# Optimization experiments

Measured on AMD Instinct MI355X. Metric: run time of the kernel, lower is better.

Reference implementation:

```python
import jax, jax.numpy as jnp
import numpy as np

B, T, N = 16, 1024, 512

def setup_inputs() -> dict:
    key = jax.random.key(0)
    ks = jax.random.split(key, 6)
    scale = 1.0 / np.sqrt(N)
    x = jax.random.normal(ks[0], (B, T, N), dtype=jnp.float32)
    Wq = jax.random.normal(ks[1], (N, N), dtype=jnp.float32) * scale
    Wk = jax.random.normal(ks[2], (N, N), dtype=jnp.float32) * scale
    Wv = jax.random.normal(ks[3], (N, N), dtype=jnp.float32) * scale
    Wp = jax.random.normal(ks[4], (N, N), dtype=jnp.float32) * scale
    bp = jnp.zeros((N,), dtype=jnp.float32)
    return {"x": x, "Wq": Wq, "Wk": Wk, "Wv": Wv, "Wp": Wp, "bp": bp}

def reference(x, Wq, Wk, Wv, Wp, bp):
    # x: [B, T, N]; conv1d(k=1) over node channels == 'oi,bit->bot' on x^T [B,N,T]
    xt = jnp.swapaxes(x, -1, -2)                     # [B, N, T]
    q = jnp.einsum('oi,bit->bot', Wq, xt)            # [B, N, T]
    k = jnp.einsum('oi,bit->bot', Wk, xt)
    v = jnp.einsum('oi,bit->bot', Wv, xt)
    n = x.shape[-1]
    attn = jnp.einsum('bnt,bmt->bnm', q, k) * (n ** -0.5)  # [B, N, N]
    attn = jax.nn.softmax(attn, axis=-1)
    px = jnp.einsum('bnm,bmt->bnt', attn, v)         # [B, N, T]
    px = jnp.swapaxes(px, -1, -2)                    # [B, T, N]
    out = jnp.einsum('btn,on->bto', px, Wp) + bp     # Linear(N,N)
    return out
```

## Files before the change

kernel.cpp:

```cpp
#include <hip/hip_runtime.h>
#include <stdint.h>

#define BB 16
#define TT 1024
#define NN 512

typedef unsigned short u16;
typedef __bf16 bf16_t;
typedef bf16_t bf16x8 __attribute__((ext_vector_type(8)));
typedef float f32x4 __attribute__((ext_vector_type(4)));

struct alignas(8) U16x4 { u16 x, y, z, w; };
struct alignas(16) F32x4 { float x, y, z, w; };

__device__ __forceinline__ u16 f2bf(float f) {
    union { float f; uint32_t u; } v; v.f = f;
    uint32_t r = v.u + 0x7fffu + ((v.u >> 16) & 1u);
    return (u16)(r >> 16);
}

__device__ __forceinline__ void gload_lds16(const void* g, void* l) {
    __builtin_amdgcn_global_load_lds(
        (const __attribute__((address_space(1))) void*)g,
        (__attribute__((address_space(3))) void*)l, 16, 0, 0);
}

__device__ __forceinline__ void xcd_swizzle(int gx, int gy, int& bx, int& by) {
    const int nwg  = gx * gy;
    const int orig = by * gx + bx;
    const int q = nwg >> 3, r = nwg & 7;
    const int xcd = orig & 7, loc = orig >> 3;
    const int swz = (xcd < r ? xcd * (q + 1) : r * (q + 1) + (xcd - r) * q) + loc;
    bx = swz % gx;
    by = swz / gx;
}

__global__ __launch_bounds__(256)
void cvt_x(const float* __restrict__ x, u16* __restrict__ xb, u16* __restrict__ xT)
{
    __shared__ u16 tile[64][70];
    const int b  = blockIdx.z;
    const int t0 = blockIdx.x * 64;
    const int n0 = blockIdx.y * 64;
    const int i  = threadIdx.x;
#pragma unroll
    for (int rep = 0; rep < 4; rep++) {
        const int lin = rep * 256 + i;
        const int r = lin >> 4, c4 = (lin & 15) * 4;
        const long src = ((long)(b * TT + t0 + r)) * NN + n0 + c4;
        F32x4 f = *(const F32x4*)&x[src];
        U16x4 u;
        u.x = f2bf(f.x); u.y = f2bf(f.y); u.z = f2bf(f.z); u.w = f2bf(f.w);
        *(U16x4*)&xb[src] = u;
        tile[r][c4] = u.x; tile[r][c4 + 1] = u.y; tile[r][c4 + 2] = u.z; tile[r][c4 + 3] = u.w;
    }
    __syncthreads();
#pragma unroll
    for (int rep = 0; rep < 4; rep++) {
        const int lin = rep * 256 + i;
        const int n = lin >> 4, t4 = (lin & 15) * 4;
        U16x4 u;
        u.x = tile[t4][n]; u.y = tile[t4 + 1][n]; u.z = tile[t4 + 2][n]; u.w = tile[t4 + 3][n];
        *(U16x4*)&xT[((long)(b * NN + n0 + n)) * TT + t0 + t4] = u;
    }
}

__global__ __launch_bounds__(256)
void cvt_w(const float* __restrict__ Wq, const float* __restrict__ Wk,
           const float* __restrict__ Wv, const float* __restrict__ Wp,
           u16* __restrict__ wb)
{
    __shared__ u16 tile[64][70];
    const int z  = blockIdx.z;
    const int r0 = blockIdx.x * 64;
    const int c0 = blockIdx.y * 64;
    const int i  = threadIdx.x;
    const float* src = (z == 0) ? Wq : (z == 1) ? Wk : (z == 2) ? Wv : Wp;
    u16* dst = wb + z * 262144;
    if (z != 2) {
#pragma unroll
        for (int rep = 0; rep < 4; rep++) {
            const int lin = rep * 256 + i;
            const int r = lin >> 4, c4 = (lin & 15) * 4;
            F32x4 f = *(const F32x4*)&src[(r0 + r) * 512 + c0 + c4];
            U16x4 u;
            u.x = f2bf(f.x); u.y = f2bf(f.y); u.z = f2bf(f.z); u.w = f2bf(f.w);
            *(U16x4*)&dst[(r0 + r) * 512 + c0 + c4] = u;
        }
    } else {
#pragma unroll
        for (int rep = 0; rep < 4; rep++) {
            const int lin = rep * 256 + i;
            const int r = lin >> 4, c4 = (lin & 15) * 4;
            F32x4 f = *(const F32x4*)&src[(r0 + r) * 512 + c0 + c4];
            tile[r][c4]     = f2bf(f.x); tile[r][c4 + 1] = f2bf(f.y);
            tile[r][c4 + 2] = f2bf(f.z); tile[r][c4 + 3] = f2bf(f.w);
        }
        __syncthreads();
#pragma unroll
        for (int rep = 0; rep < 4; rep++) {
            const int lin = rep * 256 + i;
            const int n = lin >> 4, t4 = (lin & 15) * 4;
            U16x4 u;
            u.x = tile[t4][n]; u.y = tile[t4 + 1][n]; u.z = tile[t4 + 2][n]; u.w = tile[t4 + 3][n];
            *(U16x4*)&dst[(c0 + n) * 512 + r0 + t4] = u;
        }
    }
}

template<int MODE>
__global__ __launch_bounds__(256)
void gemm_nt(const u16* __restrict__ Ag, const u16* __restrict__ Bg,
             void* __restrict__ Cg, const float* __restrict__ bias,
             int Nc, int K, int lda, int ldb,
             long sA, long sB, long sC)
{
    const u16* A  = Ag + (long)blockIdx.z * sA;
    const u16* Bt = Bg + (long)blockIdx.z * sB;

    __shared__ u16 As[2][4096];
    __shared__ u16 Bs[2][4096];

    int bx = blockIdx.x, by = blockIdx.y;
    xcd_swizzle(gridDim.x, gridDim.y, bx, by);

    const int tid  = threadIdx.x;
    const int wave = tid >> 6;
    const int lane = tid & 63;
    const int arow0 = by * 128;
    const int brow0 = bx * 128;
    const int wr = (wave >> 1) * 64;
    const int wc = (wave & 1) * 64;

    const int srow = tid >> 2;
    const int sf   = ((srow >> 1) & 3) << 4;
    const int gcol = ((tid & 3) << 4) ^ sf;
    const char* Asrc = (const char*)A  + (long)(arow0 + srow) * lda * 2 + gcol;
    const char* Bsrc = (const char*)Bt + (long)(brow0 + srow) * ldb * 2 + gcol;
    const long rstepA = (long)64 * lda * 2;
    const long rstepB = (long)64 * ldb * 2;

    f32x4 zero = {0.f, 0.f, 0.f, 0.f};
    f32x4 acc[4][4];
#pragma unroll
    for (int i = 0; i < 4; i++)
#pragma unroll
        for (int j = 0; j < 4; j++) acc[i][j] = zero;

    const int kTiles = K >> 5;

    auto stage = [&](int buf, int kt) {
        const long kb = (long)kt * 64;
        char* ad = (char*)As + buf * 8192 + tid * 16;
        char* bd = (char*)Bs + buf * 8192 + tid * 16;
        gload_lds16(Asrc + kb,          ad);
        gload_lds16(Bsrc + kb,          bd);
        gload_lds16(Asrc + rstepA + kb, ad + 4096);
        gload_lds16(Bsrc + rstepB + kb, bd + 4096);
    };

    stage(0, 0);
    int cur = 0;
    const int kbyte = (lane >> 4) << 4;
    const int rA = lane & 15;

    for (int kt = 0; kt < kTiles; ++kt) {
        if (kt + 1 < kTiles) {
            stage(cur ^ 1, kt + 1);
            asm volatile("s_waitcnt vmcnt(4)" ::: "memory");
        } else {
            asm volatile("s_waitcnt vmcnt(0)" ::: "memory");
        }
        __builtin_amdgcn_s_barrier();
        asm volatile("" ::: "memory");

        bf16x8 av[4], bv[4];
        const char* as = (const char*)As + cur * 8192;
        const char* bs = (const char*)Bs + cur * 8192;
#pragma unroll
        for (int m = 0; m < 4; m++) {
            const int row = wr + m * 16 + rA;
            av[m] = *(const bf16x8*)(as + row * 64 + (kbyte ^ (((row >> 1) & 3) << 4)));
        }
#pragma unroll
        for (int n = 0; n < 4; n++) {
            const int row = wc + n * 16 + rA;
            bv[n] = *(const bf16x8*)(bs + row * 64 + (kbyte ^ (((row >> 1) & 3) << 4)));
        }
#pragma unroll
        for (int m = 0; m < 4; m++)
#pragma unroll
            for (int n = 0; n < 4; n++)
                acc[m][n] = __builtin_amdgcn_mfma_f32_16x16x32_bf16(av[m], bv[n], acc[m][n], 0, 0, 0);

        asm volatile("" ::: "memory");
        __builtin_amdgcn_s_barrier();
        cur ^= 1;
    }

    const int r0 = (lane >> 4) << 2;
    const int cl = lane & 15;
#pragma unroll
    for (int m = 0; m < 4; m++) {
        const long gm = (long)arow0 + wr + m * 16 + r0;
#pragma unroll
        for (int n = 0; n < 4; n++) {
            const long gn = (long)brow0 + wc + n * 16 + cl;
            if (MODE == 0) {
                u16* O = (u16*)Cg + blockIdx.z * sC;
#pragma unroll
                for (int r = 0; r < 4; r++)
                    O[(gm + r) * Nc + gn] = f2bf(acc[m][n][r]);
            } else {
                float* O = (float*)Cg + blockIdx.z * sC;
                const float bb = (MODE == 3) ? bias[gn] : 0.f;
#pragma unroll
                for (int r = 0; r < 4; r++)
                    O[(gm + r) * Nc + gn] = acc[m][n][r] + bb;
            }
        }
    }
}

__global__ __launch_bounds__(256)
void softmax_rows(float* __restrict__ S)
{
    const long r = blockIdx.x;
    float* row = S + r * 512;
    const int t = threadIdx.x;
    const int lane = t & 63, wave = t >> 6;
    const float scale = 0.04419417382415922f;

    float a = row[t] * scale;
    float b = row[t + 256] * scale;

    float m = fmaxf(a, b);
#pragma unroll
    for (int o = 32; o; o >>= 1) m = fmaxf(m, __shfl_xor(m, o, 64));

    __shared__ float red[8];
    if (lane == 0) red[wave] = m;
    __syncthreads();
    m = fmaxf(fmaxf(red[0], red[1]), fmaxf(red[2], red[3]));

    float e0 = __expf(a - m), e1 = __expf(b - m);
    float s = e0 + e1;
#pragma unroll
    for (int o = 32; o; o >>= 1) s += __shfl_xor(s, o, 64);
    if (lane == 0) red[wave + 4] = s;
    __syncthreads();
    s = red[4] + red[5] + red[6] + red[7];
    const float inv = 1.f / s;

    u16* P = (u16*)row;
    P[t]       = f2bf(e0 * inv);
    P[t + 256] = f2bf(e1 * inv);
}

extern "C" void kernel_launch(void* const* d_in, const int* in_sizes, int n_in,
                              void* d_out, int out_size, void* d_ws, size_t ws_size,
                              hipStream_t stream)
{
    (void)in_sizes; (void)n_in; (void)out_size; (void)ws_size;
    const float* x  = (const float*)d_in[0];
    const float* Wq = (const float*)d_in[1];
    const float* Wk = (const float*)d_in[2];
    const float* Wv = (const float*)d_in[3];
    const float* Wp = (const float*)d_in[4];
    const float* bp = (const float*)d_in[5];
    float* out = (float*)d_out;

    char* ws = (char*)d_ws;
    size_t o = 0;
    auto alloc = [&](size_t bytes) {
        char* p = ws + o;
        o = (o + bytes + 255) & ~(size_t)255;
        return p;
    };
    u16* xb = (u16*)alloc((size_t)BB * TT * NN * 2);
    u16* xT = (u16*)alloc((size_t)BB * NN * TT * 2);
    u16* wb = (u16*)alloc((size_t)4 * NN * NN * 2);
    u16* G  = (u16*)alloc((size_t)BB * NN * NN * 2);
    u16* H  = (u16*)alloc((size_t)BB * NN * NN * 2);
    float* S = (float*)alloc((size_t)BB * NN * NN * 4);
    u16* R  = (u16*)alloc((size_t)BB * NN * NN * 2);
    u16* px = (u16*)alloc((size_t)BB * TT * NN * 2);

    const u16* wqb  = wb;
    const u16* wkb  = wb + 1 * 262144;
    const u16* wvtb = wb + 2 * 262144;
    const u16* wpb  = wb + 3 * 262144;
    const long NSQ = (long)NN * NN;

    cvt_x<<<dim3(16, 8, 16), dim3(256), 0, stream>>>(x, xb, xT);
    cvt_w<<<dim3(8, 8, 4),  dim3(256), 0, stream>>>(Wq, Wk, Wv, Wp, wb);

    const dim3 blk(256);

    gemm_nt<0><<<dim3(4, 4, 16), blk, 0, stream>>>(xT, xT, G, nullptr,
        NN, TT, TT, TT, (long)NN * TT, (long)NN * TT, NSQ);

    gemm_nt<0><<<dim3(4, 4, 16), blk, 0, stream>>>(wqb, G, H, nullptr,
        NN, NN, NN, NN, 0, NSQ, NSQ);

    gemm_nt<2><<<dim3(4, 4, 16), blk, 0, stream>>>(H, wkb, S, nullptr,
        NN, NN, NN, NN, NSQ, 0, NSQ);

    softmax_rows<<<dim3(BB * NN), blk, 0, stream>>>(S);

    gemm_nt<0><<<dim3(4, 4, 16), blk, 0, stream>>>((const u16*)S, wvtb, R, nullptr,
        NN, NN, 1024, NN, (long)NN * 1024, 0, NSQ);

    gemm_nt<0><<<dim3(4, 8, 16), blk, 0, stream>>>(xb, R, px, nullptr,
        NN, NN, NN, NN, (long)TT * NN, NSQ, (long)TT * NN);

    gemm_nt<3><<<dim3(4, 128, 1), blk, 0, stream>>>(px, wpb, out, bp,
        NN, NN, NN, NN, 0, 0, 0);
}
```

Measured before the change: 199.4 us.

## Fold output projection into per-batch weight chain, triple-buffer GEMM, fuse conversions

Result: faster. 195.3 us (-2.0%).

```diff
diff --git a/kernel.cpp b/kernel.cpp
--- a/kernel.cpp
+++ b/kernel.cpp
@@ -36,65 +36,27 @@
 }
 
 __global__ __launch_bounds__(256)
-void cvt_x(const float* __restrict__ x, u16* __restrict__ xb, u16* __restrict__ xT)
+void cvt_fused(const float* __restrict__ x,
+               const float* __restrict__ Wq, const float* __restrict__ Wk,
+               const float* __restrict__ Wv, const float* __restrict__ Wp,
+               u16* __restrict__ xb, u16* __restrict__ xT, u16* __restrict__ wb)
 {
     __shared__ u16 tile[64][70];
-    const int b  = blockIdx.z;
-    const int t0 = blockIdx.x * 64;
-    const int n0 = blockIdx.y * 64;
-    const int i  = threadIdx.x;
-#pragma unroll
-    for (int rep = 0; rep < 4; rep++) {
-        const int lin = rep * 256 + i;
-        const int r = lin >> 4, c4 = (lin & 15) * 4;
-        const long src = ((long)(b * TT + t0 + r)) * NN + n0 + c4;
-        F32x4 f = *(const F32x4*)&x[src];
-        U16x4 u;
-        u.x = f2bf(f.x); u.y = f2bf(f.y); u.z = f2bf(f.z); u.w = f2bf(f.w);
-        *(U16x4*)&xb[src] = u;
-        tile[r][c4] = u.x; tile[r][c4 + 1] = u.y; tile[r][c4 + 2] = u.z; tile[r][c4 + 3] = u.w;
-    }
-    __syncthreads();
-#pragma unroll
-    for (int rep = 0; rep < 4; rep++) {
-        const int lin = rep * 256 + i;
-        const int n = lin >> 4, t4 = (lin & 15) * 4;
-        U16x4 u;
-        u.x = tile[t4][n]; u.y = tile[t4 + 1][n]; u.z = tile[t4 + 2][n]; u.w = tile[t4 + 3][n];
-        *(U16x4*)&xT[((long)(b * NN + n0 + n)) * TT + t0 + t4] = u;
-    }
-}
-
-__global__ __launch_bounds__(256)
-void cvt_w(const float* __restrict__ Wq, const float* __restrict__ Wk,
-           const float* __restrict__ Wv, const float* __restrict__ Wp,
-           u16* __restrict__ wb)
-{
-    __shared__ u16 tile[64][70];
-    const int z  = blockIdx.z;
-    const int r0 = blockIdx.x * 64;
-    const int c0 = blockIdx.y * 64;
-    const int i  = threadIdx.x;
-    const float* src = (z == 0) ? Wq : (z == 1) ? Wk : (z == 2) ? Wv : Wp;
-    u16* dst = wb + z * 262144;
-    if (z != 2) {
+    const int i = threadIdx.x;
+    if (blockIdx.z < 16) {
+        const int b  = blockIdx.z;
+        const int t0 = blockIdx.x * 64;
+        const int n0 = blockIdx.y * 64;
 #pragma unroll
         for (int rep = 0; rep < 4; rep++) {
             const int lin = rep * 256 + i;
             const int r = lin >> 4, c4 = (lin & 15) * 4;
-            F32x4 f = *(const F32x4*)&src[(r0 + r) * 512 + c0 + c4];
+            const long src = ((long)(b * TT + t0 + r)) * NN + n0 + c4;
+            F32x4 f = *(const F32x4*)&x[src];
             U16x4 u;
             u.x = f2bf(f.x); u.y = f2bf(f.y); u.z = f2bf(f.z); u.w = f2bf(f.w);
-            *(U16x4*)&dst[(r0 + r) * 512 + c0 + c4] = u;
-        }
-    } else {
-#pragma unroll
-        for (int rep = 0; rep < 4; rep++) {
-            const int lin = rep * 256 + i;
-            const int r = lin >> 4, c4 = (lin & 15) * 4;
-            F32x4 f = *(const F32x4*)&src[(r0 + r) * 512 + c0 + c4];
-            tile[r][c4]     = f2bf(f.x); tile[r][c4 + 1] = f2bf(f.y);
-            tile[r][c4 + 2] = f2bf(f.z); tile[r][c4 + 3] = f2bf(f.w);
+            *(U16x4*)&xb[src] = u;
+            tile[r][c4] = u.x; tile[r][c4 + 1] = u.y; tile[r][c4 + 2] = u.z; tile[r][c4 + 3] = u.w;
         }
         __syncthreads();
 #pragma unroll
@@ -103,7 +65,42 @@
             const int n = lin >> 4, t4 = (lin & 15) * 4;
             U16x4 u;
             u.x = tile[t4][n]; u.y = tile[t4 + 1][n]; u.z = tile[t4 + 2][n]; u.w = tile[t4 + 3][n];
-            *(U16x4*)&dst[(c0 + n) * 512 + r0 + t4] = u;
+            *(U16x4*)&xT[((long)(b * NN + n0 + n)) * TT + t0 + t4] = u;
+        }
+    } else {
+        const int idx = (blockIdx.z - 16) * 128 + blockIdx.y * 16 + blockIdx.x;
+        const int w = idx >> 6, wt = idx & 63;
+        const int r0 = (wt >> 3) * 64, c0 = (wt & 7) * 64;
+        const float* src = (w == 0) ? Wq : (w == 1) ? Wk : (w == 2) ? Wv : Wp;
+        u16* dst = wb + w * 262144;
+        if (w != 2) {
+#pragma unroll
+            for (int rep = 0; rep < 4; rep++) {
+                const int lin = rep * 256 + i;
+                const int r = lin >> 4, c4 = (lin & 15) * 4;
+                F32x4 f = *(const F32x4*)&src[(r0 + r) * 512 + c0 + c4];
+                U16x4 u;
+                u.x = f2bf(f.x); u.y = f2bf(f.y); u.z = f2bf(f.z); u.w = f2bf(f.w);
+                *(U16x4*)&dst[(r0 + r) * 512 + c0 + c4] = u;
+            }
+        } else {
+#pragma unroll
+            for (int rep = 0; rep < 4; rep++) {
+                const int lin = rep * 256 + i;
+                const int r = lin >> 4, c4 = (lin & 15) * 4;
+                F32x4 f = *(const F32x4*)&src[(r0 + r) * 512 + c0 + c4];
+                tile[r][c4]     = f2bf(f.x); tile[r][c4 + 1] = f2bf(f.y);
+                tile[r][c4 + 2] = f2bf(f.z); tile[r][c4 + 3] = f2bf(f.w);
+            }
+            __syncthreads();
+#pragma unroll
+            for (int rep = 0; rep < 4; rep++) {
+                const int lin = rep * 256 + i;
+                const int n = lin >> 4, t4 = (lin & 15) * 4;
+                U16x4 u;
+                u.x = tile[t4][n]; u.y = tile[t4 + 1][n]; u.z = tile[t4 + 2][n]; u.w = tile[t4 + 3][n];
+                *(U16x4*)&dst[(c0 + n) * 512 + r0 + t4] = u;
+            }
         }
     }
 }
@@ -118,8 +115,8 @@
     const u16* A  = Ag + (long)blockIdx.z * sA;
     const u16* Bt = Bg + (long)blockIdx.z * sB;
 
-    __shared__ u16 As[2][4096];
-    __shared__ u16 Bs[2][4096];
+    __shared__ u16 As[3][4096];
+    __shared__ u16 Bs[3][4096];
 
     int bx = blockIdx.x, by = blockIdx.y;
     xcd_swizzle(gridDim.x, gridDim.y, bx, by);
@@ -160,13 +157,16 @@
     };
 
     stage(0, 0);
-    int cur = 0;
+    stage(1, 1);
+    int cur = 0, nxt2 = 2;
     const int kbyte = (lane >> 4) << 4;
     const int rA = lane & 15;
 
     for (int kt = 0; kt < kTiles; ++kt) {
-        if (kt + 1 < kTiles) {
-            stage(cur ^ 1, kt + 1);
+        if (kt + 2 < kTiles) {
+            stage(nxt2, kt + 2);
+            asm volatile("s_waitcnt vmcnt(8)" ::: "memory");
+        } else if (kt + 1 < kTiles) {
             asm volatile("s_waitcnt vmcnt(4)" ::: "memory");
         } else {
             asm volatile("s_waitcnt vmcnt(0)" ::: "memory");
@@ -195,7 +195,8 @@
 
         asm volatile("" ::: "memory");
         __builtin_amdgcn_s_barrier();
-        cur ^= 1;
+        cur = (cur == 2) ? 0 : cur + 1;
+        nxt2 = (nxt2 == 2) ? 0 : nxt2 + 1;
     }
 
     const int r0 = (lane >> 4) << 2;
@@ -283,8 +284,8 @@
     u16* G  = (u16*)alloc((size_t)BB * NN * NN * 2);
     u16* H  = (u16*)alloc((size_t)BB * NN * NN * 2);
     float* S = (float*)alloc((size_t)BB * NN * NN * 4);
-    u16* R  = (u16*)alloc((size_t)BB * NN * NN * 2);
-    u16* px = (u16*)alloc((size_t)BB * TT * NN * 2);
+    u16* Rt = (u16*)alloc((size_t)BB * NN * NN * 2);
+    u16* Z  = (u16*)alloc((size_t)BB * NN * NN * 2);
 
     const u16* wqb  = wb;
     const u16* wkb  = wb + 1 * 262144;
@@ -292,8 +293,7 @@
     const u16* wpb  = wb + 3 * 262144;
     const long NSQ = (long)NN * NN;
 
-    cvt_x<<<dim3(16, 8, 16), dim3(256), 0, stream>>>(x, xb, xT);
-    cvt_w<<<dim3(8, 8, 4),  dim3(256), 0, stream>>>(Wq, Wk, Wv, Wp, wb);
+    cvt_fused<<<dim3(16, 8, 18), dim3(256), 0, stream>>>(x, Wq, Wk, Wv, Wp, xb, xT, wb);
 
     const dim3 blk(256);
 
@@ -308,12 +308,12 @@
 
     softmax_rows<<<dim3(BB * NN), blk, 0, stream>>>(S);
 
-    gemm_nt<0><<<dim3(4, 4, 16), blk, 0, stream>>>((const u16*)S, wvtb, R, nullptr,
-        NN, NN, 1024, NN, (long)NN * 1024, 0, NSQ);
-
-    gemm_nt<0><<<dim3(4, 8, 16), blk, 0, stream>>>(xb, R, px, nullptr,
+    gemm_nt<0><<<dim3(4, 4, 16), blk, 0, stream>>>(wvtb, (const u16*)S, Rt, nullptr,
+        NN, NN, NN, 1024, 0, (long)NN * 1024, NSQ);
+
+    gemm_nt<0><<<dim3(4, 4, 16), blk, 0, stream>>>(wpb, Rt, Z, nullptr,
+        NN, NN, NN, NN, 0, NSQ, NSQ);
+
+    gemm_nt<3><<<dim3(4, 8, 16), blk, 0, stream>>>(xb, Z, out, bp,
         NN, NN, NN, NN, (long)TT * NN, NSQ, (long)TT * NN);
-
-    gemm_nt<3><<<dim3(4, 128, 1), blk, 0, stream>>>(px, wpb, out, bp,
-        NN, NN, NN, NN, 0, 0, 0);
-}
+}
```
